# Optimization experiments

Hardware: AMD Instinct MI355X
Metric: run time of the kernel (lower is better)

Reference implementation:

```python
import jax, jax.numpy as jnp
import numpy as np

MS_KS = 9
C = 256
BN_EPS = 1e-5


def setup_inputs() -> dict:
    key = jax.random.key(0)
    k1, k2, k3 = jax.random.split(key, 3)
    p2_r = jax.random.normal(k1, (2, C, 64, 128), dtype=jnp.float32)
    conv_w = jax.random.normal(k2, (C, C, 1, MS_KS), dtype=jnp.float32) * 0.02
    conv1_w = jax.random.normal(k3, (1, C, 1, 1), dtype=jnp.float32) * 0.05
    bn_gamma = jnp.ones((1,), jnp.float32)
    bn_beta = jnp.zeros((1,), jnp.float32)
    return dict(p2_r=p2_r, conv_w=conv_w, conv1_w=conv1_w,
                bn_gamma=bn_gamma, bn_beta=bn_beta)


def _scnn_pass(x, M):
    # x: [b,c,h,w]. Each step applies conv(1,ms_ks) to a width-1 column with
    # zero padding ms_ks//2 -> only the center tap contributes, i.e. a 256x256
    # channel matmul per column, followed by relu and residual add.
    cols = jnp.moveaxis(x, 3, 0)  # [w,b,c,h]
    def step(carry, col):
        new = col + jax.nn.relu(jnp.einsum('oc,bch->boh', M, carry))
        return new, new
    _, outs = jax.lax.scan(step, cols[0], cols[1:])
    outs = jnp.concatenate([cols[:1], outs], axis=0)[::-1]  # mirrors out[::-1]
    return jnp.moveaxis(outs, 0, 3)


def _upsample_bilinear_ac(x, factor=4):
    # F.interpolate(mode='bilinear', align_corners=True)
    b, c, h, w = x.shape
    Ho, Wo = factor * h, factor * w
    ys = jnp.arange(Ho, dtype=x.dtype) * ((h - 1) / (Ho - 1))
    xs = jnp.arange(Wo, dtype=x.dtype) * ((w - 1) / (Wo - 1))
    y0 = jnp.floor(ys).astype(jnp.int32)
    y1 = jnp.minimum(y0 + 1, h - 1)
    wy = (ys - y0.astype(x.dtype))[None, None, :, None]
    rows = x[:, :, y0, :] * (1 - wy) + x[:, :, y1, :] * wy  # [b,c,Ho,w]
    x0 = jnp.floor(xs).astype(jnp.int32)
    x1 = jnp.minimum(x0 + 1, w - 1)
    wx = (xs - x0.astype(x.dtype))[None, None, None, :]
    return rows[:, :, :, x0] * (1 - wx) + rows[:, :, :, x1] * wx


def reference(p2_r, conv_w, conv1_w, bn_gamma, bn_beta):
    M = conv_w[:, :, 0, MS_KS // 2]  # center tap, [c_out, c_in]
    x = _scnn_pass(p2_r, M)                     # reverse=False
    x = _scnn_pass(x[:, :, :, ::-1], M)         # reverse=True (slices[::-1])
    x = _upsample_bilinear_ac(x, 4)             # [b,256,4h,4w]
    x = jnp.einsum('oc,bchw->bohw', conv1_w[:, :, 0, 0], x)  # 1x1 conv -> 1 ch
    # BatchNorm2d(1), training-mode batch statistics (biased variance)
    mean = jnp.mean(x, axis=(0, 2, 3), keepdims=True)
    var = jnp.mean((x - mean) ** 2, axis=(0, 2, 3), keepdims=True)
    x = (x - mean) * jax.lax.rsqrt(var + BN_EPS)
    x = x * bn_gamma[None, :, None, None] + bn_beta[None, :, None, None]
    return jax.nn.sigmoid(x)
```

## Files before the change

kernel.cpp:

```cpp
#include <hip/hip_runtime.h>


typedef _Float16 h2 __attribute__((ext_vector_type(2)));

static __device__ __forceinline__ float fdot2(h2 a, h2 b, float c) {
#if __has_builtin(__builtin_amdgcn_fdot2)
  return __builtin_amdgcn_fdot2(a, b, c, false);
#else
  return c + (float)a.x * (float)b.x + (float)a.y * (float)b.y;
#endif
}

extern "C" __global__ void k_extract(const float* __restrict__ convw,
                                     _Float16* __restrict__ Md) {
  int idx = blockIdx.x * 256 + threadIdx.x;
  Md[idx] = (_Float16)convw[idx * 9 + 4];
}

struct SM1 {
  _Float16 cy[256] __attribute__((aligned(16)));
  _Float16 cz[256] __attribute__((aligned(16)));
  float    py[8 * 256];
  float    pz[8 * 256];
  float    sp[128 * 4];
};

extern "C" __global__ void __launch_bounds__(512, 2)
k_scan(const float* __restrict__ p2, const _Float16* __restrict__ Md,
       const float* __restrict__ conv1, float* __restrict__ sout,
       float* __restrict__ stats) {
  __shared__ SM1 sm;
  const int tid  = threadIdx.x;
  const int lane = tid & 63;
  const int r    = tid >> 6;
  const int b    = blockIdx.x >> 6;
  const int h    = blockIdx.x & 63;

  if (blockIdx.x == 0 && tid == 0) { stats[0] = 0.f; stats[1] = 0.f; }

  h2 M[4][16];
#pragma unroll
  for (int i = 0; i < 4; ++i) {
    const uint4* mp = (const uint4*)(Md + ((lane * 4 + i) * 256 + r * 32));
#pragma unroll
    for (int j = 0; j < 4; ++j) {
      uint4 d = mp[j];
      M[i][j * 4 + 0] = __builtin_bit_cast(h2, d.x);
      M[i][j * 4 + 1] = __builtin_bit_cast(h2, d.y);
      M[i][j * 4 + 2] = __builtin_bit_cast(h2, d.z);
      M[i][j * 4 + 3] = __builtin_bit_cast(h2, d.w);
    }
  }

  const float* pbase = p2 + (((size_t)b * 256) * 64 + h) * 128;

  float vreg = 0.f, cnext = 0.f;
  if (tid < 256) {
    vreg = conv1[tid];
    float c0 = pbase[(size_t)tid * 8192 + 0];
    cnext    = pbase[(size_t)tid * 8192 + 1];
    sm.cy[tid] = (_Float16)c0;
    sm.cz[tid] = (_Float16)c0;
    float val = vreg * c0;
#pragma unroll
    for (int off = 32; off > 0; off >>= 1) val += __shfl_xor(val, off, 64);
    if (lane == 0) sm.sp[0 * 4 + r] = val;
  }
  __syncthreads();

  const uint4* cy4 = (const uint4*)sm.cy + r * 4;
  const uint4* cz4 = (const uint4*)sm.cz + r * 4;
  float4* pyw = (float4*)(sm.py + r * 256 + lane * 4);
  float4* pzw = (float4*)(sm.pz + r * 256 + lane * 4);

  for (int w = 1; w < 128; ++w) {
    uint4 Y[4], Z[4];
#pragma unroll
    for (int j = 0; j < 4; ++j) { Y[j] = cy4[j]; Z[j] = cz4[j]; }
    h2 yv[16], zv[16];
#pragma unroll
    for (int j = 0; j < 4; ++j) {
      yv[j * 4 + 0] = __builtin_bit_cast(h2, Y[j].x);
      yv[j * 4 + 1] = __builtin_bit_cast(h2, Y[j].y);
      yv[j * 4 + 2] = __builtin_bit_cast(h2, Y[j].z);
      yv[j * 4 + 3] = __builtin_bit_cast(h2, Y[j].w);
      zv[j * 4 + 0] = __builtin_bit_cast(h2, Z[j].x);
      zv[j * 4 + 1] = __builtin_bit_cast(h2, Z[j].y);
      zv[j * 4 + 2] = __builtin_bit_cast(h2, Z[j].z);
      zv[j * 4 + 3] = __builtin_bit_cast(h2, Z[j].w);
    }
    float ay0 = 0.f, ay1 = 0.f, ay2 = 0.f, ay3 = 0.f;
    float az0 = 0.f, az1 = 0.f, az2 = 0.f, az3 = 0.f;
#pragma unroll
    for (int k = 0; k < 16; ++k) {
      ay0 = fdot2(M[0][k], yv[k], ay0);
      ay1 = fdot2(M[1][k], yv[k], ay1);
      ay2 = fdot2(M[2][k], yv[k], ay2);
      ay3 = fdot2(M[3][k], yv[k], ay3);
      az0 = fdot2(M[0][k], zv[k], az0);
      az1 = fdot2(M[1][k], zv[k], az1);
      az2 = fdot2(M[2][k], zv[k], az2);
      az3 = fdot2(M[3][k], zv[k], az3);
    }
    *pyw = make_float4(ay0, ay1, ay2, ay3);
    *pzw = make_float4(az0, az1, az2, az3);
    __syncthreads();

    if (tid < 256) {
      float cw = cnext;
      if (w < 127) cnext = pbase[(size_t)tid * 8192 + w + 1];
      float sy = 0.f, sz = 0.f;
#pragma unroll
      for (int rr = 0; rr < 8; ++rr) {
        sy += sm.py[rr * 256 + tid];
        sz += sm.pz[rr * 256 + tid];
      }
      float yn = cw + fmaxf(sy, 0.f);
      float zn = yn + fmaxf(sz, 0.f);
      sm.cy[tid] = (_Float16)yn;
      sm.cz[tid] = (_Float16)zn;
      float val = vreg * zn;
#pragma unroll
      for (int off = 32; off > 0; off >>= 1) val += __shfl_xor(val, off, 64);
      if (lane == 0) sm.sp[w * 4 + r] = val;
    }
    __syncthreads();
  }

  if (tid < 128) {
    float sv = sm.sp[tid * 4 + 0] + sm.sp[tid * 4 + 1] +
               sm.sp[tid * 4 + 2] + sm.sp[tid * 4 + 3];
    sout[(blockIdx.x << 7) + (127 - tid)] = sv;
  }
}

static __device__ __forceinline__ float bilin(const float* __restrict__ s,
                                              int idx) {
  int bb  = idx >> 17;
  int rem = idx & 131071;
  int ho  = rem >> 9;
  int wo  = rem & 511;
  const float SY = 63.0f / 255.0f, SX = 127.0f / 511.0f;
  float fy = (float)ho * SY;
  int y0 = (int)fy; int y1 = min(y0 + 1, 63); float wy = fy - (float)y0;
  float fx = (float)wo * SX;
  int x0 = (int)fx; int x1 = min(x0 + 1, 127); float wx = fx - (float)x0;
  const float* sb = s + bb * 8192;
  float cA = sb[y0 * 128 + x0] * (1.f - wy) + sb[y1 * 128 + x0] * wy;
  float cB = sb[y0 * 128 + x1] * (1.f - wy) + sb[y1 * 128 + x1] * wy;
  return cA * (1.f - wx) + cB * wx;
}

extern "C" __global__ void k_stats(const float* __restrict__ s,
                                   float* __restrict__ stats) {
  int tid  = threadIdx.x;
  int base = blockIdx.x * 1024 + tid;
  float sum = 0.f, ssq = 0.f;
#pragma unroll
  for (int i = 0; i < 4; ++i) {
    float u = bilin(s, base + i * 256);
    sum += u; ssq += u * u;
  }
#pragma unroll
  for (int off = 32; off > 0; off >>= 1) {
    sum += __shfl_xor(sum, off, 64);
    ssq += __shfl_xor(ssq, off, 64);
  }
  __shared__ float ls[4], lq[4];
  int wv = tid >> 6;
  if ((tid & 63) == 0) { ls[wv] = sum; lq[wv] = ssq; }
  __syncthreads();
  if (tid == 0) {
    atomicAdd(&stats[0], ls[0] + ls[1] + ls[2] + ls[3]);
    atomicAdd(&stats[1], lq[0] + lq[1] + lq[2] + lq[3]);
  }
}

extern "C" __global__ void k_norm(const float* __restrict__ s,
                                  const float* __restrict__ stats,
                                  const float* __restrict__ gamma,
                                  const float* __restrict__ beta,
                                  float* __restrict__ out) {
  int tid  = threadIdx.x;
  int base = blockIdx.x * 1024 + tid;
  const float invN = 1.f / 262144.f;
  float mean  = stats[0] * invN;
  float var   = stats[1] * invN - mean * mean;
  float scale = rsqrtf(var + 1e-5f) * gamma[0];
  float bias  = beta[0] - mean * scale;
#pragma unroll
  for (int i = 0; i < 4; ++i) {
    int idx = base + i * 256;
    float u = bilin(s, idx);
    float x = u * scale + bias;
    out[idx] = 1.f / (1.f + __expf(-x));
  }
}

extern "C" void kernel_launch(void* const* d_in, const int* in_sizes, int n_in,
                              void* d_out, int out_size, void* d_ws, size_t ws_size,
                              hipStream_t stream) {
  const float* p2    = (const float*)d_in[0];
  const float* convw = (const float*)d_in[1];
  const float* conv1 = (const float*)d_in[2];
  const float* gamma = (const float*)d_in[3];
  const float* beta  = (const float*)d_in[4];
  float* out = (float*)d_out;

  char* ws = (char*)d_ws;
  float*    s     = (float*)ws;
  float*    stats = (float*)(ws + 65536);
  _Float16* Md    = (_Float16*)(ws + 65792);

  hipLaunchKernelGGL(k_extract, dim3(256), dim3(256), 0, stream, convw, Md);
  hipLaunchKernelGGL(k_scan,    dim3(128), dim3(512), 0, stream, p2, Md, conv1, s, stats);
  hipLaunchKernelGGL(k_stats,   dim3(256), dim3(256), 0, stream, s, stats);
  hipLaunchKernelGGL(k_norm,    dim3(256), dim3(256), 0, stream, s, stats, gamma, beta, out);
}
```

Measured before the change: 212.2 us.

## Use MFMA 16x16x32 f16 for per-column recurrence with double-buffered state

Replaces the scalar fdot2 per-column matvec with MFMA instructions. The Y and Z state vectors are packed as two columns of the B operand, so one wave computes 32 output channels without a cross-wave partial-sum reduction. Double-buffered state in shared memory cuts the loop to a single barrier per step, and the Y result is passed to the Z lanes by shuffle. The extract kernel now reads convw with vectorized loads. The cost is that 14 of the 16 MFMA columns are unused, and the Z update uses Y rounded to fp16.

```diff
diff --git a/kernel.cpp b/kernel.cpp
--- a/kernel.cpp
+++ b/kernel.cpp
@@ -1,136 +1,165 @@
 #include <hip/hip_runtime.h>
 
 
-typedef _Float16 h2 __attribute__((ext_vector_type(2)));
-
-static __device__ __forceinline__ float fdot2(h2 a, h2 b, float c) {
-#if __has_builtin(__builtin_amdgcn_fdot2)
-  return __builtin_amdgcn_fdot2(a, b, c, false);
-#else
-  return c + (float)a.x * (float)b.x + (float)a.y * (float)b.y;
-#endif
-}
+typedef _Float16 f16x8 __attribute__((ext_vector_type(8)));
+typedef _Float16 f16x4 __attribute__((ext_vector_type(4)));
+typedef float    f32x4 __attribute__((ext_vector_type(4)));
 
 extern "C" __global__ void k_extract(const float* __restrict__ convw,
                                      _Float16* __restrict__ Md) {
-  int idx = blockIdx.x * 256 + threadIdx.x;
-  Md[idx] = (_Float16)convw[idx * 9 + 4];
-}
-
-struct SM1 {
-  _Float16 cy[256] __attribute__((aligned(16)));
-  _Float16 cz[256] __attribute__((aligned(16)));
-  float    py[8 * 256];
-  float    pz[8 * 256];
-  float    sp[128 * 4];
+  int q = blockIdx.x * 256 + threadIdx.x;
+  float4 v = ((const float4*)convw)[q];
+  float vv[4] = {v.x, v.y, v.z, v.w};
+  int f = q * 4;
+#pragma unroll
+  for (int e = 0; e < 4; ++e) {
+    int flat = f + e;
+    if (flat % 9 == 4) Md[flat / 9] = (_Float16)vv[e];
+  }
+}
+
+struct SM {
+  _Float16 cy[2][256];
+  _Float16 cz[2][256];
+  float    sp[128 * 32];
 };
 
 extern "C" __global__ void __launch_bounds__(512, 2)
 k_scan(const float* __restrict__ p2, const _Float16* __restrict__ Md,
        const float* __restrict__ conv1, float* __restrict__ sout,
        float* __restrict__ stats) {
-  __shared__ SM1 sm;
+  __shared__ SM sm;
   const int tid  = threadIdx.x;
-  const int lane = tid & 63;
+  const int l    = tid & 63;
   const int r    = tid >> 6;
+  const int col  = l & 15;
+  const int quad = l >> 4;
   const int b    = blockIdx.x >> 6;
   const int h    = blockIdx.x & 63;
 
   if (blockIdx.x == 0 && tid == 0) { stats[0] = 0.f; stats[1] = 0.f; }
 
-  h2 M[4][16];
-#pragma unroll
-  for (int i = 0; i < 4; ++i) {
-    const uint4* mp = (const uint4*)(Md + ((lane * 4 + i) * 256 + r * 32));
-#pragma unroll
-    for (int j = 0; j < 4; ++j) {
-      uint4 d = mp[j];
-      M[i][j * 4 + 0] = __builtin_bit_cast(h2, d.x);
-      M[i][j * 4 + 1] = __builtin_bit_cast(h2, d.y);
-      M[i][j * 4 + 2] = __builtin_bit_cast(h2, d.z);
-      M[i][j * 4 + 3] = __builtin_bit_cast(h2, d.w);
-    }
-  }
-
-  const float* pbase = p2 + (((size_t)b * 256) * 64 + h) * 128;
-
-  float vreg = 0.f, cnext = 0.f;
-  if (tid < 256) {
-    vreg = conv1[tid];
-    float c0 = pbase[(size_t)tid * 8192 + 0];
-    cnext    = pbase[(size_t)tid * 8192 + 1];
-    sm.cy[tid] = (_Float16)c0;
-    sm.cz[tid] = (_Float16)c0;
-    float val = vreg * c0;
-#pragma unroll
-    for (int off = 32; off > 0; off >>= 1) val += __shfl_xor(val, off, 64);
-    if (lane == 0) sm.sp[0 * 4 + r] = val;
+  const bool isY = (col == 0);
+  const bool isZ = (col == 1);
+
+  const int m0 = (r * 2 + 0) * 16 + quad * 4;
+  const int m1 = (r * 2 + 1) * 16 + quad * 4;
+
+  f16x8 A0[8], A1[8];
+#pragma unroll
+  for (int ch = 0; ch < 8; ++ch) {
+    A0[ch] = *(const f16x8*)(Md + ((r*2+0)*16 + col) * 256 + ch*32 + quad*8);
+    A1[ch] = *(const f16x8*)(Md + ((r*2+1)*16 + col) * 256 + ch*32 + quad*8);
+  }
+
+  const float* pbase = p2 + (size_t)b * 2097152 + (size_t)h * 128;
+
+  float vva[4], vvb[4];
+  {
+    float c0a[4], c0b[4];
+    if (isY || isZ) {
+#pragma unroll
+      for (int i = 0; i < 4; ++i) {
+        c0a[i] = pbase[(size_t)(m0 + i) * 8192];
+        c0b[i] = pbase[(size_t)(m1 + i) * 8192];
+      }
+    }
+    if (isY) {
+      f16x4 pa, pb;
+#pragma unroll
+      for (int i = 0; i < 4; ++i) { pa[i] = (_Float16)c0a[i]; pb[i] = (_Float16)c0b[i]; }
+      *(f16x4*)(sm.cy[0] + m0) = pa; *(f16x4*)(sm.cy[0] + m1) = pb;
+      *(f16x4*)(sm.cz[0] + m0) = pa; *(f16x4*)(sm.cz[0] + m1) = pb;
+    }
+    if (isZ) {
+#pragma unroll
+      for (int i = 0; i < 4; ++i) { vva[i] = conv1[m0 + i]; vvb[i] = conv1[m1 + i]; }
+      float p = 0.f;
+#pragma unroll
+      for (int i = 0; i < 4; ++i) p += vva[i] * c0a[i] + vvb[i] * c0b[i];
+      sm.sp[0 * 32 + r * 4 + quad] = p;
+    }
+  }
+
+  float ca[4], cb[4];
+  if (isY) {
+#pragma unroll
+    for (int i = 0; i < 4; ++i) {
+      ca[i] = pbase[(size_t)(m0 + i) * 8192 + 1];
+      cb[i] = pbase[(size_t)(m1 + i) * 8192 + 1];
+    }
   }
   __syncthreads();
 
-  const uint4* cy4 = (const uint4*)sm.cy + r * 4;
-  const uint4* cz4 = (const uint4*)sm.cz + r * 4;
-  float4* pyw = (float4*)(sm.py + r * 256 + lane * 4);
-  float4* pzw = (float4*)(sm.pz + r * 256 + lane * 4);
+  const _Float16* selA = ((l & 1) ? sm.cz[0] : sm.cy[0]) + quad * 8;
+  const _Float16* selB = ((l & 1) ? sm.cz[1] : sm.cy[1]) + quad * 8;
 
   for (int w = 1; w < 128; ++w) {
-    uint4 Y[4], Z[4];
-#pragma unroll
-    for (int j = 0; j < 4; ++j) { Y[j] = cy4[j]; Z[j] = cz4[j]; }
-    h2 yv[16], zv[16];
-#pragma unroll
-    for (int j = 0; j < 4; ++j) {
-      yv[j * 4 + 0] = __builtin_bit_cast(h2, Y[j].x);
-      yv[j * 4 + 1] = __builtin_bit_cast(h2, Y[j].y);
-      yv[j * 4 + 2] = __builtin_bit_cast(h2, Y[j].z);
-      yv[j * 4 + 3] = __builtin_bit_cast(h2, Y[j].w);
-      zv[j * 4 + 0] = __builtin_bit_cast(h2, Z[j].x);
-      zv[j * 4 + 1] = __builtin_bit_cast(h2, Z[j].y);
-      zv[j * 4 + 2] = __builtin_bit_cast(h2, Z[j].z);
-      zv[j * 4 + 3] = __builtin_bit_cast(h2, Z[j].w);
-    }
-    float ay0 = 0.f, ay1 = 0.f, ay2 = 0.f, ay3 = 0.f;
-    float az0 = 0.f, az1 = 0.f, az2 = 0.f, az3 = 0.f;
-#pragma unroll
-    for (int k = 0; k < 16; ++k) {
-      ay0 = fdot2(M[0][k], yv[k], ay0);
-      ay1 = fdot2(M[1][k], yv[k], ay1);
-      ay2 = fdot2(M[2][k], yv[k], ay2);
-      ay3 = fdot2(M[3][k], yv[k], ay3);
-      az0 = fdot2(M[0][k], zv[k], az0);
-      az1 = fdot2(M[1][k], zv[k], az1);
-      az2 = fdot2(M[2][k], zv[k], az2);
-      az3 = fdot2(M[3][k], zv[k], az3);
-    }
-    *pyw = make_float4(ay0, ay1, ay2, ay3);
-    *pzw = make_float4(az0, az1, az2, az3);
+    float na[4], nb[4];
+    if (isY && w < 127) {
+#pragma unroll
+      for (int i = 0; i < 4; ++i) {
+        na[i] = pbase[(size_t)(m0 + i) * 8192 + w + 1];
+        nb[i] = pbase[(size_t)(m1 + i) * 8192 + w + 1];
+      }
+    }
+
+    const _Float16* sel = (w & 1) ? selA : selB;
+    f16x8 B[8];
+#pragma unroll
+    for (int ch = 0; ch < 8; ++ch)
+      B[ch] = *(const f16x8*)(sel + ch * 32);
+
+    f32x4 acc0 = {0.f, 0.f, 0.f, 0.f}, acc1 = {0.f, 0.f, 0.f, 0.f};
+#pragma unroll
+    for (int ch = 0; ch < 8; ++ch) {
+      acc0 = __builtin_amdgcn_mfma_f32_16x16x32_f16(A0[ch], B[ch], acc0, 0, 0, 0);
+      acc1 = __builtin_amdgcn_mfma_f32_16x16x32_f16(A1[ch], B[ch], acc1, 0, 0, 0);
+    }
+
+    _Float16* wy = sm.cy[w & 1];
+    _Float16* wz = sm.cz[w & 1];
+    f16x4 yh0 = {}, yh1 = {};
+    if (isY) {
+#pragma unroll
+      for (int i = 0; i < 4; ++i) {
+        yh0[i] = (_Float16)(ca[i] + fmaxf(acc0[i], 0.f));
+        yh1[i] = (_Float16)(cb[i] + fmaxf(acc1[i], 0.f));
+      }
+      *(f16x4*)(wy + m0) = yh0;
+      *(f16x4*)(wy + m1) = yh1;
+    }
+    int2 u0 = __builtin_bit_cast(int2, yh0), u1 = __builtin_bit_cast(int2, yh1);
+    u0.x = __shfl(u0.x, l & 62, 64); u0.y = __shfl(u0.y, l & 62, 64);
+    u1.x = __shfl(u1.x, l & 62, 64); u1.y = __shfl(u1.y, l & 62, 64);
+    f16x4 ys0 = __builtin_bit_cast(f16x4, u0), ys1 = __builtin_bit_cast(f16x4, u1);
+    if (isZ) {
+      f16x4 zh0, zh1;
+      float p = 0.f;
+#pragma unroll
+      for (int i = 0; i < 4; ++i) {
+        float z0 = (float)ys0[i] + fmaxf(acc0[i], 0.f);
+        float z1 = (float)ys1[i] + fmaxf(acc1[i], 0.f);
+        zh0[i] = (_Float16)z0; zh1[i] = (_Float16)z1;
+        p += vva[i] * z0 + vvb[i] * z1;
+      }
+      *(f16x4*)(wz + m0) = zh0;
+      *(f16x4*)(wz + m1) = zh1;
+      sm.sp[w * 32 + r * 4 + quad] = p;
+    }
+    if (isY) {
+#pragma unroll
+      for (int i = 0; i < 4; ++i) { ca[i] = na[i]; cb[i] = nb[i]; }
+    }
     __syncthreads();
-
-    if (tid < 256) {
-      float cw = cnext;
-      if (w < 127) cnext = pbase[(size_t)tid * 8192 + w + 1];
-      float sy = 0.f, sz = 0.f;
-#pragma unroll
-      for (int rr = 0; rr < 8; ++rr) {
-        sy += sm.py[rr * 256 + tid];
-        sz += sm.pz[rr * 256 + tid];
-      }
-      float yn = cw + fmaxf(sy, 0.f);
-      float zn = yn + fmaxf(sz, 0.f);
-      sm.cy[tid] = (_Float16)yn;
-      sm.cz[tid] = (_Float16)zn;
-      float val = vreg * zn;
-#pragma unroll
-      for (int off = 32; off > 0; off >>= 1) val += __shfl_xor(val, off, 64);
-      if (lane == 0) sm.sp[w * 4 + r] = val;
-    }
-    __syncthreads();
   }
 
   if (tid < 128) {
-    float sv = sm.sp[tid * 4 + 0] + sm.sp[tid * 4 + 1] +
-               sm.sp[tid * 4 + 2] + sm.sp[tid * 4 + 3];
-    sout[(blockIdx.x << 7) + (127 - tid)] = sv;
+    const float4* q = (const float4*)(sm.sp + tid * 32);
+    float s = 0.f;
+#pragma unroll
+    for (int j = 0; j < 8; ++j) { float4 t4 = q[j]; s += t4.x + t4.y + t4.z + t4.w; }
+    sout[(blockIdx.x << 7) + (127 - tid)] = s;
   }
 }
 
@@ -212,7 +241,7 @@
   float*    stats = (float*)(ws + 65536);
   _Float16* Md    = (_Float16*)(ws + 65792);
 
-  hipLaunchKernelGGL(k_extract, dim3(256), dim3(256), 0, stream, convw, Md);
+  hipLaunchKernelGGL(k_extract, dim3(576), dim3(256), 0, stream, convw, Md);
   hipLaunchKernelGGL(k_scan,    dim3(128), dim3(512), 0, stream, p2, Md, conv1, s, stats);
   hipLaunchKernelGGL(k_stats,   dim3(256), dim3(256), 0, stream, s, stats);
   hipLaunchKernelGGL(k_norm,    dim3(256), dim3(256), 0, stream, s, stats, gamma, beta, out);
```

Measured after the change: 201.5 us. -5.0%, faster.
